# Kernel tuning notes

Measured on AMD Instinct MI355X. Metric: run time of the kernel, lower is better.

## Reference

```python
import jax, jax.numpy as jnp
import numpy as np
import math

NUM_LEAD = 12
PATCHES = 100  # patch_num_v * patch_num_h = 5 * 20
HEADS = 12
HID = 768
DH = HID // HEADS  # 64
SEQ = NUM_LEAD * PATCHES + NUM_LEAD + 1  # 1213
INTER = 3072
BATCH = 8


def _layer_norm(x, g, b, eps=1e-12):
    u = x.mean(-1, keepdims=True)
    s = ((x - u) ** 2).mean(-1, keepdims=True)
    return g * (x - u) / jnp.sqrt(s + eps) + b


def _lead_mask():
    # make_mask with fusion == 0: additive bias applied to query rows [0, NUM_LEAD+1)
    cols = jnp.arange(SEQ)
    # CLS row: 1 at lead-token positions 1..NUM_LEAD
    cls_row = jnp.where((cols >= 1) & (cols < NUM_LEAD + 1), 1.0, 0.0)
    # Lead rows: 1 everywhere except own patch block
    i = jnp.arange(NUM_LEAD)[:, None]
    start = NUM_LEAD + 1 + PATCHES * i
    in_block = (cols[None, :] >= start) & (cols[None, :] < start + PATCHES)
    lead_rows = jnp.where(in_block, 0.0, 1.0)
    mask = jnp.concatenate([cls_row[None, :], lead_rows], axis=0)  # [NUM_LEAD+1, SEQ]
    return mask * (-99999.0)


def setup_inputs() -> dict:
    key = jax.random.key(0)
    ks = jax.random.split(key, 12)
    std = 0.02
    d = {
        "hidden_states": jax.random.normal(ks[0], (BATCH, SEQ, HID), jnp.float32),
        "attention_mask": jnp.zeros((BATCH, 1, 1, SEQ), jnp.float32),
        "Wq": jax.random.normal(ks[1], (HID, HID), jnp.float32) * std,
        "bq": jnp.zeros((HID,), jnp.float32),
        "Wk": jax.random.normal(ks[2], (HID, HID), jnp.float32) * std,
        "bk": jnp.zeros((HID,), jnp.float32),
        "Wv": jax.random.normal(ks[3], (HID, HID), jnp.float32) * std,
        "bv": jnp.zeros((HID,), jnp.float32),
        "Wo": jax.random.normal(ks[4], (HID, HID), jnp.float32) * std,
        "bo": jnp.zeros((HID,), jnp.float32),
        "gamma1": jnp.ones((HID,), jnp.float32),
        "beta1": jnp.zeros((HID,), jnp.float32),
        "Wi": jax.random.normal(ks[5], (HID, INTER), jnp.float32) * std,
        "bi": jnp.zeros((INTER,), jnp.float32),
        "Wd": jax.random.normal(ks[6], (INTER, HID), jnp.float32) * std,
        "bd": jnp.zeros((HID,), jnp.float32),
        "gamma2": jnp.ones((HID,), jnp.float32),
        "beta2": jnp.zeros((HID,), jnp.float32),
    }
    return d


def reference(hidden_states, attention_mask, Wq, bq, Wk, bk, Wv, bv, Wo, bo,
              gamma1, beta1, Wi, bi, Wd, bd, gamma2, beta2):
    B, S, _ = hidden_states.shape

    def heads(x):  # [B,S,HID] -> [B,H,S,DH]
        return x.reshape(B, S, HEADS, DH).transpose(0, 2, 1, 3)

    q = heads(hidden_states @ Wq + bq)
    k = heads(hidden_states @ Wk + bk)
    v = heads(hidden_states @ Wv + bv)

    scores = jnp.einsum("bhqd,bhkd->bhqk", q, k) / math.sqrt(DH)
    scores = scores + attention_mask  # broadcast [B,1,1,S]
    lead_mask = _lead_mask()  # [NUM_LEAD+1, SEQ]
    scores = scores.at[:, :, : NUM_LEAD + 1, :].add(lead_mask[None, None])

    probs = jax.nn.softmax(scores, axis=-1)  # dropout is identity in eval
    ctx = jnp.einsum("bhqk,bhkd->bhqd", probs, v)
    ctx = ctx.transpose(0, 2, 1, 3).reshape(B, S, HID)

    attn_out = _layer_norm(ctx @ Wo + bo + hidden_states, gamma1, beta1)
    inter = jax.nn.gelu(attn_out @ Wi + bi, approximate=False)  # exact erf gelu
    out = _layer_norm(inter @ Wd + bd + attn_out, gamma2, beta2)
    return out
```

## Files before the change

### kernel.cpp

```cpp
#include <hip/hip_runtime.h>
#include <hip/hip_bf16.h>
#include <stdint.h>

typedef unsigned short u16;
typedef unsigned int u32;
typedef __attribute__((ext_vector_type(8))) short frag8;
typedef __attribute__((ext_vector_type(4))) float f32x4;

#define SEQ 1213
#define BATCH 8
#define HEADS 12
#define DH 64
#define HID 768
#define INTER 3072
#define BS (BATCH*SEQ)

#define MFMA(a,b,c) __builtin_amdgcn_mfma_f32_16x16x32_bf16(a,b,c,0,0,0)

__device__ __forceinline__ float b2f(u16 u){ u32 i=((u32)u)<<16; float f; __builtin_memcpy(&f,&i,4); return f; }
__device__ __forceinline__ u16 f2b(float f){ u32 i; __builtin_memcpy(&i,&f,4); i = i + 0x7fffu + ((i>>16)&1u); return (u16)(i>>16); }
__device__ __forceinline__ u32 pack2(float a, float b){ return (u32)f2b(a) | ((u32)f2b(b)<<16); }

__device__ __forceinline__ void async16(const u16* g, u16* l){
  __builtin_amdgcn_global_load_lds((const __attribute__((address_space(1))) u32*)(uintptr_t)g,
                                   (__attribute__((address_space(3))) u32*)(uintptr_t)l, 16, 0, 0);
}

__global__ __launch_bounds__(256) void convert_arr(const void* __restrict__ src,
  u16* __restrict__ dst, int n8, const u16* __restrict__ probe)
{
  const bool f32 = (probe[0] == 0);
  int i = blockIdx.x*256 + threadIdx.x;
  if (i >= n8) return;
  u16 tmp[8];
  if (f32){
    const float* s = (const float*)src + (size_t)i*8;
#pragma unroll
    for (int j=0;j<8;j++) tmp[j] = f2b(s[j]);
  } else {
    *(uint4*)tmp = *((const uint4*)src + i);
  }
  *((uint4*)dst + i) = *(const uint4*)tmp;
}

__global__ __launch_bounds__(256) void convert_small(
  const void* bq, const void* bk, const void* bv, const void* bo,
  const void* bi, const void* bd, const void* g1, const void* be1,
  const void* g2, const void* be2, const void* am,
  u16* __restrict__ dst, const u16* __restrict__ probe)
{
  const int starts[12] = {0,768,1536,2304,3072,6144,6912,7680,8448,9216,9984,19688};
  const void* srcs[11] = {bq,bk,bv,bo,bi,bd,g1,be1,g2,be2,am};
  const bool f32 = (probe[0] == 0);
  int e = (blockIdx.x*256 + threadIdx.x) * 8;
  if (e >= 19688) return;
  int seg = 0;
#pragma unroll
  for (int k=1;k<11;k++) if (starts[k] <= e) seg = k;
  int off = e - starts[seg];
  const void* s = srcs[seg];
  u16 tmp[8];
  if (f32){
    const float* sf = (const float*)s + off;
#pragma unroll
    for (int j=0;j<8;j++) tmp[j] = f2b(sf[j]);
  } else {
    const u16* sh = (const u16*)s + off;
#pragma unroll
    for (int j=0;j<8;j++) tmp[j] = sh[j];
  }
  *(uint4*)(dst + e) = *(const uint4*)tmp;
}

__global__ __launch_bounds__(256) void transpose2(const void* __restrict__ in,
  u16* __restrict__ out, int R, int C, const u16* __restrict__ probe)
{
  const bool f32 = (probe[0] == 0);
  __shared__ u16 tile[32][33];
  const int bx = blockIdx.x*32, by = blockIdx.y*32;
  const int tx = threadIdx.x & 31, ty = threadIdx.x >> 5;
  if (f32){
    const float* inf_ = (const float*)in;
#pragma unroll
    for (int i=ty;i<32;i+=8) tile[i][tx] = f2b(inf_[(size_t)(by+i)*C + bx+tx]);
  } else {
    const u16* inh = (const u16*)in;
#pragma unroll
    for (int i=ty;i<32;i+=8) tile[i][tx] = inh[(size_t)(by+i)*C + bx+tx];
  }
  __syncthreads();
#pragma unroll
  for (int i=ty;i<32;i+=8) out[(size_t)(bx+i)*R + by+tx] = tile[tx][i];
}

__device__ __forceinline__ void gemm_tile(
    const u16* __restrict__ A, const u16* __restrict__ BT,
    int M, int K, int m0, int n0,
    u16* ldsA, u16* ldsB, f32x4 acc[4][4])
{
  const int t = threadIdx.x;
  const int w = t >> 6, l = t & 63;
  const int lw = l & 15, lh = l >> 4;
  const int rowo = (w >> 1) << 6;
  const int colo = (w & 1) << 6;
  const int sr  = t >> 2;
  const int sc8 = (t & 3) << 3;
  int ra = m0 + sr;      if (ra >= M) ra = M - 1;
  int rb = m0 + sr + 64; if (rb >= M) rb = M - 1;
  const u16* Ap0 = A + (size_t)ra*K + sc8;
  const u16* Ap1 = A + (size_t)rb*K + sc8;
  const u16* Bp0 = BT + (size_t)(n0+sr)*K + sc8;
  const u16* Bp1 = BT + (size_t)(n0+sr+64)*K + sc8;
  u16* lA0 = ldsA + sr*32 + sc8;
  u16* lA1 = ldsA + (sr+64)*32 + sc8;
  u16* lB0 = ldsB + sr*32 + sc8;
  u16* lB1 = ldsB + (sr+64)*32 + sc8;

  for (int k0 = 0; k0 < K; k0 += 32) {
    __syncthreads();
    async16(Ap0 + k0, lA0);
    async16(Ap1 + k0, lA1);
    async16(Bp0 + k0, lB0);
    async16(Bp1 + k0, lB1);
    __syncthreads();
    frag8 af[4], bf[4];
#pragma unroll
    for (int mi=0;mi<4;mi++) af[mi] = *(const frag8*)(ldsA + (rowo + mi*16 + lw)*32 + lh*8);
#pragma unroll
    for (int ni=0;ni<4;ni++) bf[ni] = *(const frag8*)(ldsB + (colo + ni*16 + lw)*32 + lh*8);
#pragma unroll
    for (int mi=0;mi<4;mi++)
#pragma unroll
      for (int ni=0;ni<4;ni++)
        acc[mi][ni] = MFMA(af[mi], bf[ni], acc[mi][ni]);
  }
}

__global__ __launch_bounds__(256,2) void gemm_qkv(
  const u16* __restrict__ A, const u16* __restrict__ BT,
  const u16* __restrict__ bq, const u16* __restrict__ bk, const u16* __restrict__ bv,
  u16* __restrict__ Qo, u16* __restrict__ Ko, u16* __restrict__ Vo)
{
  __shared__ __align__(16) u16 ldsA[128*32];
  __shared__ __align__(16) u16 ldsB[128*32];
  f32x4 acc[4][4];
#pragma unroll
  for (int i=0;i<4;i++)
#pragma unroll
    for (int j=0;j<4;j++) acc[i][j] = 0.f;
  const int m0 = blockIdx.x*128, n0 = blockIdx.y*128;
  gemm_tile(A, BT, BS, HID, m0, n0, ldsA, ldsB, acc);
  const int t=threadIdx.x, w=t>>6, l=t&63, lw=l&15, lh=l>>4;
  const int rowb = m0 + ((w>>1)<<6), colb = n0 + ((w&1)<<6);
#pragma unroll
  for (int ni=0;ni<4;ni++){
    int cc = colb + ni*16 + lw;
    int which = cc / HID;
    int n2 = cc - which*HID;
    int h = n2 >> 6, d = n2 & 63;
    const u16* bp = which==0 ? bq : (which==1 ? bk : bv);
    u16* op = which==0 ? Qo : (which==1 ? Ko : Vo);
    float bias = b2f(bp[n2]);
    float scale = which==0 ? 0.125f : 1.0f;
#pragma unroll
    for (int mi=0;mi<4;mi++){
#pragma unroll
      for (int r=0;r<4;r++){
        int rr = rowb + mi*16 + lh*4 + r;
        if (rr < BS){
          int bi_ = rr / SEQ;
          int si  = rr - bi_*SEQ;
          float v = (acc[mi][ni][r] + bias) * scale;
          op[(((size_t)(bi_*HEADS + h))*SEQ + si)*64 + d] = f2b(v);
        }
      }
    }
  }
}

__global__ __launch_bounds__(256,2) void gemm_resid(
  const u16* __restrict__ A, const u16* __restrict__ BT,
  const u16* __restrict__ bias, const u16* __restrict__ resid,
  u16* __restrict__ out, int N, int K)
{
  __shared__ __align__(16) u16 ldsA[128*32];
  __shared__ __align__(16) u16 ldsB[128*32];
  f32x4 acc[4][4];
#pragma unroll
  for (int i=0;i<4;i++)
#pragma unroll
    for (int j=0;j<4;j++) acc[i][j] = 0.f;
  const int m0 = blockIdx.x*128, n0 = blockIdx.y*128;
  gemm_tile(A, BT, BS, K, m0, n0, ldsA, ldsB, acc);
  const int t=threadIdx.x, w=t>>6, l=t&63, lw=l&15, lh=l>>4;
  const int rowb = m0 + ((w>>1)<<6), colb = n0 + ((w&1)<<6);
#pragma unroll
  for (int ni=0;ni<4;ni++){
    int cc = colb + ni*16 + lw;
    float bv_ = b2f(bias[cc]);
#pragma unroll
    for (int mi=0;mi<4;mi++){
#pragma unroll
      for (int r=0;r<4;r++){
        int rr = rowb + mi*16 + lh*4 + r;
        if (rr < BS){
          float v = acc[mi][ni][r] + bv_ + b2f(resid[(size_t)rr*N + cc]);
          out[(size_t)rr*N + cc] = f2b(v);
        }
      }
    }
  }
}

__global__ __launch_bounds__(256,2) void gemm_gelu(
  const u16* __restrict__ A, const u16* __restrict__ BT,
  const u16* __restrict__ bias, u16* __restrict__ out, int N, int K)
{
  __shared__ __align__(16) u16 ldsA[128*32];
  __shared__ __align__(16) u16 ldsB[128*32];
  f32x4 acc[4][4];
#pragma unroll
  for (int i=0;i<4;i++)
#pragma unroll
    for (int j=0;j<4;j++) acc[i][j] = 0.f;
  const int m0 = blockIdx.x*128, n0 = blockIdx.y*128;
  gemm_tile(A, BT, BS, K, m0, n0, ldsA, ldsB, acc);
  const int t=threadIdx.x, w=t>>6, l=t&63, lw=l&15, lh=l>>4;
  const int rowb = m0 + ((w>>1)<<6), colb = n0 + ((w&1)<<6);
#pragma unroll
  for (int ni=0;ni<4;ni++){
    int cc = colb + ni*16 + lw;
    float bv_ = b2f(bias[cc]);
#pragma unroll
    for (int mi=0;mi<4;mi++){
#pragma unroll
      for (int r=0;r<4;r++){
        int rr = rowb + mi*16 + lh*4 + r;
        if (rr < BS){
          float v = acc[mi][ni][r] + bv_;
          v = 0.5f * v * (1.0f + erff(v * 0.70710678118654752f));
          out[(size_t)rr*N + cc] = f2b(v);
        }
      }
    }
  }
}

__global__ __launch_bounds__(256,4) void attn_kernel(
  const u16* __restrict__ Qb, const u16* __restrict__ Kb, const u16* __restrict__ Vb,
  const u16* __restrict__ amask, u16* __restrict__ ctx)
{
  __shared__ __align__(16) u16 sQP[64*72];
  __shared__ __align__(16) u16 sK[64*72];
  __shared__ __align__(16) u16 sV[64*72];
  __shared__ float sEm[64];
  const int t = threadIdx.x, w = t>>6, l = t&63, lw = l&15, lh = l>>4;
  const int bh = blockIdx.y, b = bh / HEADS;
  const int q0 = blockIdx.x * 64;
  const int h = bh % HEADS;
  const size_t hb = (size_t)bh * SEQ * 64;
  const u16* Qp = Qb + hb;
  const u16* Kp = Kb + hb;
  const u16* Vp = Vb + hb;

  {
    int r = t >> 3, c = t & 7;
#pragma unroll
    for (int i=0;i<2;i++){
      int rr = i*32 + r;
      int s = q0 + rr; if (s > SEQ-1) s = SEQ-1;
      *(uint4*)(sQP + rr*72 + c*8) = *(const uint4*)(Qp + (size_t)s*64 + c*8);
    }
  }
  __syncthreads();
  frag8 qa[2];
#pragma unroll
  for (int kk=0;kk<2;kk++) qa[kk] = *(const frag8*)(sQP + (w*16 + lw)*72 + kk*32 + lh*8);
  u16* pw = sQP + w*16*72;

  float m_s = -1e30f, l_s = 0.f;
  f32x4 o[4];
#pragma unroll
  for (int i=0;i<4;i++) o[i] = 0.f;
  const bool leadwave = (q0 == 0) && (w == 0);

  const int nkt = (SEQ + 63) / 64;
  for (int kt = 0; kt < nkt; kt++) {
    const int s0 = kt * 64;
    __syncthreads();
    {
      int r = t >> 3, c = t & 7;
#pragma unroll
      for (int i=0;i<2;i++){
        int rr = i*32 + r;
        int s = s0 + rr; if (s > SEQ-1) s = SEQ-1;
        *(uint4*)(sK + rr*72 + c*8) = *(const uint4*)(Kp + (size_t)s*64 + c*8);
        uint4 vv = *(const uint4*)(Vp + (size_t)s*64 + c*8);
        const u16* vp = (const u16*)&vv;
        int scol = (((rr>>3) ^ (c&3))<<3) + (rr&7);
#pragma unroll
        for (int j=0;j<8;j++)
          sV[(c*8 + j)*72 + scol] = vp[j];
      }
      if (t < 64){
        int sg = s0 + t;
        sEm[t] = (sg < SEQ) ? __expf(b2f(amask[b*SEQ + sg])) : 0.f;
      }
    }
    __syncthreads();

    f32x4 st[4];
#pragma unroll
    for (int si=0;si<4;si++){
      f32x4 a0 = 0.f;
#pragma unroll
      for (int kk=0;kk<2;kk++){
        frag8 kf = *(const frag8*)(sK + (si*16 + lw)*72 + kk*32 + lh*8);
        a0 = MFMA(kf, qa[kk], a0);
      }
      st[si] = a0;
    }

    float mx = -1e30f;
#pragma unroll
    for (int si=0;si<4;si++)
#pragma unroll
      for (int r=0;r<4;r++) mx = fmaxf(mx, st[si][r]);
    mx = fmaxf(mx, __shfl_xor(mx, 16));
    mx = fmaxf(mx, __shfl_xor(mx, 32));
    float nm = fmaxf(m_s, mx);
    float alpha = __expf(m_s - nm);
    m_s = nm;
    float rs = 0.f;
#pragma unroll
    for (int si=0;si<4;si++){
      f32x4 emv = *(const f32x4*)(sEm + si*16 + lh*4);
#pragma unroll
      for (int r=0;r<4;r++){
        float p = __expf(st[si][r] - nm) * emv[r];
        if (leadwave){
          int sg = s0 + si*16 + lh*4 + r;
          int q = lw;
          if (q == 0){
            if (sg >= 1 && sg < 13) p = 0.f;
          } else if (q < 13){
            int stt = 13 + 100*(q-1);
            if (!(sg >= stt && sg < stt+100)) p = 0.f;
          }
        }
        st[si][r] = p;
        rs += p;
      }
    }
    rs += __shfl_xor(rs, 16);
    rs += __shfl_xor(rs, 32);
    l_s = l_s*alpha + rs;

#pragma unroll
    for (int r=0;r<4;r++){
      float af = __shfl(alpha, (l & 48) + ((l >> 4) << 2) + r);
#pragma unroll
      for (int ni=0;ni<4;ni++) o[ni][r] *= af;
    }

#pragma unroll
    for (int si=0;si<4;si++){
      u32 p01 = pack2(st[si][0], st[si][1]);
      u32 p23 = pack2(st[si][2], st[si][3]);
      *(u32*)(pw + lw*72 + si*16 + lh*4)     = p01;
      *(u32*)(pw + lw*72 + si*16 + lh*4 + 2) = p23;
    }
    __threadfence_block();

#pragma unroll
    for (int kk=0;kk<2;kk++){
      frag8 pf = *(const frag8*)(pw + lw*72 + kk*32 + lh*8);
#pragma unroll
      for (int ni=0;ni<4;ni++){
        int d = ni*16 + lw;
        int grp = (kk*4 + lh) ^ ((d>>3) & 3);
        frag8 vf = *(const frag8*)(sV + d*72 + (grp<<3));
        o[ni] = MFMA(pf, vf, o[ni]);
      }
    }
  }

#pragma unroll
  for (int r=0;r<4;r++){
    float lf = __shfl(l_s, (l & 48) + ((l >> 4) << 2) + r);
    int qg = q0 + w*16 + lh*4 + r;
    if (qg < SEQ){
      float inv = 1.0f / lf;
#pragma unroll
      for (int ni=0;ni<4;ni++){
        ctx[((size_t)(b*SEQ) + qg)*HID + h*64 + ni*16 + lw] = f2b(o[ni][r] * inv);
      }
    }
  }
}

__global__ __launch_bounds__(256) void ln_kernel(const u16* __restrict__ y,
  const u16* __restrict__ g, const u16* __restrict__ be,
  u16* __restrict__ outb, float* __restrict__ outf)
{
  const int row = blockIdx.x, t = threadIdx.x;
  const u16* yp = y + (size_t)row*HID;
  float x0 = b2f(yp[t]), x1 = b2f(yp[t+256]), x2 = b2f(yp[t+512]);
  float s = x0 + x1 + x2;
  __shared__ float red[4];
#pragma unroll
  for (int off=1; off<64; off<<=1) s += __shfl_xor(s, off);
  if ((t & 63) == 0) red[t>>6] = s;
  __syncthreads();
  float u = (red[0]+red[1]+red[2]+red[3]) * (1.0f/768.0f);
  float d0=x0-u, d1=x1-u, d2=x2-u;
  float s2 = d0*d0 + d1*d1 + d2*d2;
  __syncthreads();
#pragma unroll
  for (int off=1; off<64; off<<=1) s2 += __shfl_xor(s2, off);
  if ((t & 63) == 0) red[t>>6] = s2;
  __syncthreads();
  float var = (red[0]+red[1]+red[2]+red[3]) * (1.0f/768.0f);
  float rstd = rsqrtf(var + 1e-12f);
  float v0 = b2f(g[t])    *(d0*rstd) + b2f(be[t]);
  float v1 = b2f(g[t+256])*(d1*rstd) + b2f(be[t+256]);
  float v2 = b2f(g[t+512])*(d2*rstd) + b2f(be[t+512]);
  if (outf){
    float* op = outf + (size_t)row*HID;
    op[t] = v0; op[t+256] = v1; op[t+512] = v2;
  } else {
    u16* op = outb + (size_t)row*HID;
    op[t] = f2b(v0); op[t+256] = f2b(v1); op[t+512] = f2b(v2);
  }
}

extern "C" void kernel_launch(void* const* d_in, const int* in_sizes, int n_in,
                              void* d_out, int out_size, void* d_ws, size_t ws_size,
                              hipStream_t stream)
{
  const void* hidden = d_in[0];
  const void* amask  = d_in[1];
  const void* Wq = d_in[2];  const void* bq = d_in[3];
  const void* Wk = d_in[4];  const void* bk = d_in[5];
  const void* Wv = d_in[6];  const void* bv = d_in[7];
  const void* Wo = d_in[8];  const void* bo = d_in[9];
  const void* g1 = d_in[10]; const void* be1= d_in[11];
  const void* Wi = d_in[12]; const void* bi = d_in[13];
  const void* Wd = d_in[14]; const void* bd = d_in[15];
  const void* g2 = d_in[16]; const void* be2= d_in[17];
  const u16* probe = (const u16*)g1;

  char* ws = (char*)d_ws;
  size_t off = 0;
  auto alloc = [&](size_t elems)->u16* {
    u16* p = (u16*)(ws + off);
    off += ((elems*2 + 255) & ~(size_t)255);
    return p;
  };
  u16* hiddenC = alloc((size_t)BS*HID);
  u16* smallC  = alloc((size_t)19688);
  u16* WqkvT = alloc((size_t)2304*768);
  u16* WoT   = alloc((size_t)768*768);
  u16* WiT   = alloc((size_t)3072*768);
  u16* WdT   = alloc((size_t)768*3072);
  u16* Qb    = alloc((size_t)BS*HID);
  u16* Kb    = alloc((size_t)BS*HID);
  u16* Vb    = alloc((size_t)BS*HID);
  u16* y1    = alloc((size_t)BS*HID);
  u16* interb = Qb;
  u16* ctxb  = alloc((size_t)BS*HID);
  u16* attn_out = alloc((size_t)BS*HID);
  u16* y2 = ctxb;

  const u16* c_bq = smallC;        const u16* c_bk = smallC+768;
  const u16* c_bv = smallC+1536;   const u16* c_bo = smallC+2304;
  const u16* c_bi = smallC+3072;   const u16* c_bd = smallC+6144;
  const u16* c_g1 = smallC+6912;   const u16* c_be1= smallC+7680;
  const u16* c_g2 = smallC+8448;   const u16* c_be2= smallC+9216;
  const u16* c_am = smallC+9984;

  dim3 blk(256);
  convert_arr<<<dim3((BS*HID/8 + 255)/256), blk, 0, stream>>>(hidden, hiddenC, BS*HID/8, probe);
  convert_small<<<dim3(10), blk, 0, stream>>>(bq,bk,bv,bo,bi,bd,g1,be1,g2,be2,amask, smallC, probe);
  transpose2<<<dim3(24,24),blk,0,stream>>>(Wq, WqkvT,              768, 768, probe);
  transpose2<<<dim3(24,24),blk,0,stream>>>(Wk, WqkvT + 768*768,    768, 768, probe);
  transpose2<<<dim3(24,24),blk,0,stream>>>(Wv, WqkvT + 2*768*768,  768, 768, probe);
  transpose2<<<dim3(24,24),blk,0,stream>>>(Wo, WoT, 768, 768, probe);
  transpose2<<<dim3(96,24),blk,0,stream>>>(Wi, WiT, 768, 3072, probe);
  transpose2<<<dim3(24,96),blk,0,stream>>>(Wd, WdT, 3072, 768, probe);

  gemm_qkv<<<dim3(76,18),blk,0,stream>>>(hiddenC, WqkvT, c_bq,c_bk,c_bv, Qb,Kb,Vb);
  attn_kernel<<<dim3(19,96),blk,0,stream>>>(Qb,Kb,Vb, c_am, ctxb);
  gemm_resid<<<dim3(76,6),blk,0,stream>>>(ctxb, WoT, c_bo, hiddenC, y1, 768, 768);
  ln_kernel<<<dim3(BS),blk,0,stream>>>(y1, c_g1, c_be1, attn_out, nullptr);
  gemm_gelu<<<dim3(76,24),blk,0,stream>>>(attn_out, WiT, c_bi, interb, 3072, 768);
  gemm_resid<<<dim3(76,6),blk,0,stream>>>(interb, WdT, c_bd, attn_out, y2, 768, 3072);
  ln_kernel<<<dim3(BS),blk,0,stream>>>(y2, c_g2, c_be2, nullptr, (float*)d_out);
}
```

Measured before the change: 553.7 us.

## Deepen GEMM K-tile to 64 with XOR-swizzled LDS, double attention query tile

The shared GEMM tile loop now stages 64-wide K slices instead of 32, using an XOR-swizzled LDS layout so fragment reads avoid bank conflicts. This halves the number of barrier pairs per K loop. The attention kernel moves to 512-thread blocks covering 128 query rows, so each K/V tile loaded into LDS serves twice as many queries. The cost is more LDS per block, lower occupancy for both kernels (attention launch bounds drop to one block), and more padded query rows at the sequence tail.

```diff
diff --git a/kernel.cpp b/kernel.cpp
--- a/kernel.cpp
+++ b/kernel.cpp
@@ -103,36 +103,42 @@
   const int lw = l & 15, lh = l >> 4;
   const int rowo = (w >> 1) << 6;
   const int colo = (w & 1) << 6;
-  const int sr  = t >> 2;
-  const int sc8 = (t & 3) << 3;
-  int ra = m0 + sr;      if (ra >= M) ra = M - 1;
-  int rb = m0 + sr + 64; if (rb >= M) rb = M - 1;
-  const u16* Ap0 = A + (size_t)ra*K + sc8;
-  const u16* Ap1 = A + (size_t)rb*K + sc8;
-  const u16* Bp0 = BT + (size_t)(n0+sr)*K + sc8;
-  const u16* Bp1 = BT + (size_t)(n0+sr+64)*K + sc8;
-  u16* lA0 = ldsA + sr*32 + sc8;
-  u16* lA1 = ldsA + (sr+64)*32 + sc8;
-  u16* lB0 = ldsB + sr*32 + sc8;
-  u16* lB1 = ldsB + (sr+64)*32 + sc8;
-
-  for (int k0 = 0; k0 < K; k0 += 32) {
+  const int srow = w*8 + (l>>3);
+  const int scol = ((l&7) ^ ((l>>3)&7)) * 8;
+
+  const u16* gpA[4]; const u16* gpB[4];
+  u16* lpA[4]; u16* lpB[4];
+#pragma unroll
+  for (int p=0;p<4;p++){
+    int ra = m0 + p*32 + srow; if (ra >= M) ra = M-1;
+    gpA[p] = A  + (size_t)ra*K + scol;
+    gpB[p] = BT + (size_t)(n0 + p*32 + srow)*K + scol;
+    lpA[p] = ldsA + (p*32 + w*8)*64 + l*8;
+    lpB[p] = ldsB + (p*32 + w*8)*64 + l*8;
+  }
+
+  const int slot0 = lw & 7;
+  for (int k0 = 0; k0 < K; k0 += 64) {
     __syncthreads();
-    async16(Ap0 + k0, lA0);
-    async16(Ap1 + k0, lA1);
-    async16(Bp0 + k0, lB0);
-    async16(Bp1 + k0, lB1);
+#pragma unroll
+    for (int p=0;p<4;p++) async16(gpA[p] + k0, lpA[p]);
+#pragma unroll
+    for (int p=0;p<4;p++) async16(gpB[p] + k0, lpB[p]);
     __syncthreads();
-    frag8 af[4], bf[4];
-#pragma unroll
-    for (int mi=0;mi<4;mi++) af[mi] = *(const frag8*)(ldsA + (rowo + mi*16 + lw)*32 + lh*8);
-#pragma unroll
-    for (int ni=0;ni<4;ni++) bf[ni] = *(const frag8*)(ldsB + (colo + ni*16 + lw)*32 + lh*8);
-#pragma unroll
-    for (int mi=0;mi<4;mi++)
-#pragma unroll
-      for (int ni=0;ni<4;ni++)
-        acc[mi][ni] = MFMA(af[mi], bf[ni], acc[mi][ni]);
+#pragma unroll
+    for (int kk=0;kk<2;kk++){
+      const int slot = ((kk*4 + lh) ^ slot0) * 8;
+      frag8 af[4], bf[4];
+#pragma unroll
+      for (int mi=0;mi<4;mi++) af[mi] = *(const frag8*)(ldsA + (rowo + mi*16 + lw)*64 + slot);
+#pragma unroll
+      for (int ni=0;ni<4;ni++) bf[ni] = *(const frag8*)(ldsB + (colo + ni*16 + lw)*64 + slot);
+#pragma unroll
+      for (int mi=0;mi<4;mi++)
+#pragma unroll
+        for (int ni=0;ni<4;ni++)
+          acc[mi][ni] = MFMA(af[mi], bf[ni], acc[mi][ni]);
+    }
   }
 }
 
@@ -141,8 +147,8 @@
   const u16* __restrict__ bq, const u16* __restrict__ bk, const u16* __restrict__ bv,
   u16* __restrict__ Qo, u16* __restrict__ Ko, u16* __restrict__ Vo)
 {
-  __shared__ __align__(16) u16 ldsA[128*32];
-  __shared__ __align__(16) u16 ldsB[128*32];
+  __shared__ __align__(16) u16 ldsA[128*64];
+  __shared__ __align__(16) u16 ldsB[128*64];
   f32x4 acc[4][4];
 #pragma unroll
   for (int i=0;i<4;i++)
@@ -183,8 +189,8 @@
   const u16* __restrict__ bias, const u16* __restrict__ resid,
   u16* __restrict__ out, int N, int K)
 {
-  __shared__ __align__(16) u16 ldsA[128*32];
-  __shared__ __align__(16) u16 ldsB[128*32];
+  __shared__ __align__(16) u16 ldsA[128*64];
+  __shared__ __align__(16) u16 ldsB[128*64];
   f32x4 acc[4][4];
 #pragma unroll
   for (int i=0;i<4;i++)
@@ -216,8 +222,8 @@
   const u16* __restrict__ A, const u16* __restrict__ BT,
   const u16* __restrict__ bias, u16* __restrict__ out, int N, int K)
 {
-  __shared__ __align__(16) u16 ldsA[128*32];
-  __shared__ __align__(16) u16 ldsB[128*32];
+  __shared__ __align__(16) u16 ldsA[128*64];
+  __shared__ __align__(16) u16 ldsB[128*64];
   f32x4 acc[4][4];
 #pragma unroll
   for (int i=0;i<4;i++)
@@ -246,17 +252,17 @@
   }
 }
 
-__global__ __launch_bounds__(256,4) void attn_kernel(
+__global__ __launch_bounds__(512,1) void attn_kernel(
   const u16* __restrict__ Qb, const u16* __restrict__ Kb, const u16* __restrict__ Vb,
   const u16* __restrict__ amask, u16* __restrict__ ctx)
 {
-  __shared__ __align__(16) u16 sQP[64*72];
+  __shared__ __align__(16) u16 sQP[128*72];
   __shared__ __align__(16) u16 sK[64*72];
   __shared__ __align__(16) u16 sV[64*72];
   __shared__ float sEm[64];
   const int t = threadIdx.x, w = t>>6, l = t&63, lw = l&15, lh = l>>4;
   const int bh = blockIdx.y, b = bh / HEADS;
-  const int q0 = blockIdx.x * 64;
+  const int q0 = blockIdx.x * 128;
   const int h = bh % HEADS;
   const size_t hb = (size_t)bh * SEQ * 64;
   const u16* Qp = Qb + hb;
@@ -267,7 +273,7 @@
     int r = t >> 3, c = t & 7;
 #pragma unroll
     for (int i=0;i<2;i++){
-      int rr = i*32 + r;
+      int rr = i*64 + r;
       int s = q0 + rr; if (s > SEQ-1) s = SEQ-1;
       *(uint4*)(sQP + rr*72 + c*8) = *(const uint4*)(Qp + (size_t)s*64 + c*8);
     }
@@ -289,19 +295,15 @@
     const int s0 = kt * 64;
     __syncthreads();
     {
-      int r = t >> 3, c = t & 7;
-#pragma unroll
-      for (int i=0;i<2;i++){
-        int rr = i*32 + r;
-        int s = s0 + rr; if (s > SEQ-1) s = SEQ-1;
-        *(uint4*)(sK + rr*72 + c*8) = *(const uint4*)(Kp + (size_t)s*64 + c*8);
-        uint4 vv = *(const uint4*)(Vp + (size_t)s*64 + c*8);
-        const u16* vp = (const u16*)&vv;
-        int scol = (((rr>>3) ^ (c&3))<<3) + (rr&7);
-#pragma unroll
-        for (int j=0;j<8;j++)
-          sV[(c*8 + j)*72 + scol] = vp[j];
-      }
+      int rr = t >> 3, c = t & 7;
+      int s = s0 + rr; if (s > SEQ-1) s = SEQ-1;
+      *(uint4*)(sK + rr*72 + c*8) = *(const uint4*)(Kp + (size_t)s*64 + c*8);
+      uint4 vv = *(const uint4*)(Vp + (size_t)s*64 + c*8);
+      const u16* vp = (const u16*)&vv;
+      int scol = (((rr>>3) ^ (c&3))<<3) + (rr&7);
+#pragma unroll
+      for (int j=0;j<8;j++)
+        sV[(c*8 + j)*72 + scol] = vp[j];
       if (t < 64){
         int sg = s0 + t;
         sEm[t] = (sg < SEQ) ? __expf(b2f(amask[b*SEQ + sg])) : 0.f;
@@ -365,10 +367,8 @@
 
 #pragma unroll
     for (int si=0;si<4;si++){
-      u32 p01 = pack2(st[si][0], st[si][1]);
-      u32 p23 = pack2(st[si][2], st[si][3]);
-      *(u32*)(pw + lw*72 + si*16 + lh*4)     = p01;
-      *(u32*)(pw + lw*72 + si*16 + lh*4 + 2) = p23;
+      *(u32*)(pw + lw*72 + si*16 + lh*4)     = pack2(st[si][0], st[si][1]);
+      *(u32*)(pw + lw*72 + si*16 + lh*4 + 2) = pack2(st[si][2], st[si][3]);
     }
     __threadfence_block();
 
@@ -490,7 +490,7 @@
   transpose2<<<dim3(24,96),blk,0,stream>>>(Wd, WdT, 3072, 768, probe);
 
   gemm_qkv<<<dim3(76,18),blk,0,stream>>>(hiddenC, WqkvT, c_bq,c_bk,c_bv, Qb,Kb,Vb);
-  attn_kernel<<<dim3(19,96),blk,0,stream>>>(Qb,Kb,Vb, c_am, ctxb);
+  attn_kernel<<<dim3(10,96),dim3(512),0,stream>>>(Qb,Kb,Vb, c_am, ctxb);
   gemm_resid<<<dim3(76,6),blk,0,stream>>>(ctxb, WoT, c_bo, hiddenC, y1, 768, 768);
   ln_kernel<<<dim3(BS),blk,0,stream>>>(y1, c_g1, c_be1, attn_out, nullptr);
   gemm_gelu<<<dim3(76,24),blk,0,stream>>>(attn_out, WiT, c_bi, interb, 3072, 768);
```

New measurement: 516.2 us. -6.8%, faster.
